# Optimization experiments

Measured on AMD Instinct MI355X. Metric: run time of the kernel, lower is better.

The kernel has to match this reference:

```python
import jax, jax.numpy as jnp
import numpy as np

N = 100000
E = 600000
D_IN, D_HID, D_OUT = 128, 128, 64


def setup_inputs() -> dict:
    key = jax.random.key(0)
    k1, k2, k3, k4 = jax.random.split(key, 4)
    x = jax.random.normal(k1, (N, D_IN), dtype=jnp.float32)
    edge_index = jax.random.randint(k2, (2, E), 0, N, dtype=jnp.int64)
    edge_weight = jnp.ones((E,), dtype=jnp.float32)
    W1 = jax.random.normal(k3, (D_IN, D_HID), dtype=jnp.float32) / np.sqrt(D_IN)
    b1 = jnp.zeros((D_HID,), dtype=jnp.float32)
    W2 = jax.random.normal(k4, (D_HID, D_OUT), dtype=jnp.float32) / np.sqrt(D_HID)
    b2 = jnp.zeros((D_OUT,), dtype=jnp.float32)
    return {"x": x, "edge_index": edge_index, "edge_weight": edge_weight,
            "W1": W1, "b1": b1, "W2": W2, "b2": b2}


def _gcn_conv(x, row, col, ew, W, b, n_nodes):
    # x: [N, d_in]; row/col/ew include self loops. PyG gcn_norm:
    # deg[i] = sum of ew over edges with target i; norm = d^-1/2[row]*ew*d^-1/2[col]
    deg = jax.ops.segment_sum(ew, col, num_segments=n_nodes)
    dinv = jnp.where(deg > 0, jax.lax.rsqrt(deg), 0.0)
    norm = dinv[row] * ew * dinv[col]  # [E+N]
    xw = x @ W  # dense transform first (d_out <= d_in path)
    msg = xw[row] * norm[:, None]  # gather + scale  [E+N, d_out]
    out = jax.ops.segment_sum(msg, col, num_segments=n_nodes)  # scatter-add
    return out + b


def reference(x, edge_index, edge_weight, W1, b1, W2, b2):
    n = x.shape[0]
    loops = jnp.arange(n, dtype=edge_index.dtype)
    row = jnp.concatenate([edge_index[0], loops])
    col = jnp.concatenate([edge_index[1], loops])
    ew = jnp.concatenate([edge_weight, jnp.ones((n,), dtype=edge_weight.dtype)])
    # dropout is identity in eval mode
    h = jax.nn.relu(_gcn_conv(x, row, col, ew, W1, b1, n))
    out = _gcn_conv(h, row, col, ew, W2, b2, n)
    return out
```

## Files before the change

kernel.cpp:

```cpp
#include <hip/hip_runtime.h>


constexpr int SCAN_BLOCKS = 256;

typedef __attribute__((ext_vector_type(8))) short short8;
typedef __attribute__((ext_vector_type(4))) float f32x4;

__device__ __forceinline__ ushort f2bf(float f) {
    unsigned u = __float_as_uint(f);
    return (ushort)((u + 0x7fffu + ((u >> 16) & 1u)) >> 16);
}
__device__ __forceinline__ float bf2f(ushort h) {
    return __uint_as_float((unsigned)h << 16);
}

__global__ __launch_bounds__(256, 2) void gemm1_kernel(
        const float* __restrict__ X, const float* __restrict__ W1,
        ushort* __restrict__ Ab, int N, int G,
        int* __restrict__ cnt, const float* __restrict__ W2,
        ushort* __restrict__ W2t) {
    __shared__ __align__(16) ushort sX[128 * 128];
    __shared__ __align__(16) ushort sW[128 * 128];
    const int tid = threadIdx.x;

    if (blockIdx.x >= G) {
        const int b = blockIdx.x - G;
        const int n4 = (N + 3) >> 2;
        const int nbz = (n4 + 255) / 256;
        if (b < nbz) {
            const int i = b * 256 + tid;
            if (i < n4) reinterpret_cast<int4*>(cnt)[i] = make_int4(0, 0, 0, 0);
        } else {
            const int o = (b - nbz) * 256 + tid;
            if (o < 64 * 128)
                W2t[o] = f2bf(W2[(size_t)(o & 127) * 64 + (o >> 7)]);
        }
        return;
    }

    const int base = blockIdx.x * 128;
    #pragma unroll
    for (int p = 0; p < 8; p++) {
        const int ch = p * 256 + tid;
        const int r = ch >> 4, cpos = ch & 15;
        const int grow = base + r;
        uint4 u = make_uint4(0, 0, 0, 0);
        if (grow < N) {
            const float* xp = X + (size_t)grow * 128 + cpos * 8;
            const float4 a = *reinterpret_cast<const float4*>(xp);
            const float4 c = *reinterpret_cast<const float4*>(xp + 4);
            u.x = (uint)f2bf(a.x) | ((uint)f2bf(a.y) << 16);
            u.y = (uint)f2bf(a.z) | ((uint)f2bf(a.w) << 16);
            u.z = (uint)f2bf(c.x) | ((uint)f2bf(c.y) << 16);
            u.w = (uint)f2bf(c.z) | ((uint)f2bf(c.w) << 16);
        }
        const int b = (cpos * 16) ^ ((r & 7) << 4);
        *reinterpret_cast<uint4*>(reinterpret_cast<char*>(sX) + r * 256 + b) = u;
    }
    #pragma unroll
    for (int p = 0; p < 8; p++) {
        const int ch = p * 256 + tid;
        const int c = ch & 127, kc = ch >> 7;
        const int k0 = kc * 8;
        float f[8];
        #pragma unroll
        for (int j = 0; j < 8; j++) f[j] = W1[(size_t)(k0 + j) * 128 + c];
        uint4 u;
        u.x = (uint)f2bf(f[0]) | ((uint)f2bf(f[1]) << 16);
        u.y = (uint)f2bf(f[2]) | ((uint)f2bf(f[3]) << 16);
        u.z = (uint)f2bf(f[4]) | ((uint)f2bf(f[5]) << 16);
        u.w = (uint)f2bf(f[6]) | ((uint)f2bf(f[7]) << 16);
        const int b = (k0 * 2) ^ ((c & 7) << 4);
        *reinterpret_cast<uint4*>(reinterpret_cast<char*>(sW) + c * 256 + b) = u;
    }
    __syncthreads();

    const int lane = tid & 63;
    const int wid = tid >> 6;
    const int wr = wid >> 1;
    const int wc = wid & 1;
    const int lr = lane & 15;
    const int g  = lane >> 4;

    f32x4 acc[4][4];
    #pragma unroll
    for (int i = 0; i < 4; i++)
        #pragma unroll
        for (int f = 0; f < 4; f++) acc[i][f] = (f32x4){0.f, 0.f, 0.f, 0.f};

    #pragma unroll
    for (int ks = 0; ks < 4; ks++) {
        const int koff = ks * 64 + g * 16;
        short8 a[4], b[4];
        #pragma unroll
        for (int i = 0; i < 4; i++) {
            const int r = wr * 64 + i * 16 + lr;
            a[i] = *reinterpret_cast<const short8*>(
                reinterpret_cast<const char*>(sX) + r * 256 + (koff ^ ((r & 7) << 4)));
        }
        #pragma unroll
        for (int f = 0; f < 4; f++) {
            const int c = wc * 64 + f * 16 + lr;
            b[f] = *reinterpret_cast<const short8*>(
                reinterpret_cast<const char*>(sW) + c * 256 + (koff ^ ((c & 7) << 4)));
        }
        #pragma unroll
        for (int i = 0; i < 4; i++)
            #pragma unroll
            for (int f = 0; f < 4; f++)
                acc[i][f] = __builtin_amdgcn_mfma_f32_16x16x32_bf16(a[i], b[f], acc[i][f], 0, 0, 0);
    }

    #pragma unroll
    for (int i = 0; i < 4; i++)
        #pragma unroll
        for (int reg = 0; reg < 4; reg++) {
            const int grow = base + wr * 64 + i * 16 + g * 4 + reg;
            if (grow < N)
                #pragma unroll
                for (int f = 0; f < 4; f++)
                    Ab[(size_t)grow * 128 + wc * 64 + f * 16 + lr] = f2bf(acc[i][f][reg]);
        }
}

__global__ void cnt_kernel(const int* __restrict__ col, int* __restrict__ cnt,
                           int* __restrict__ rank, int E) {
    const int T = gridDim.x * blockDim.x;
    for (int e = blockIdx.x * blockDim.x + threadIdx.x; e < E; e += T)
        rank[e] = atomicAdd(&cnt[col[e]], 1);
}

__global__ __launch_bounds__(256) void scan_part_kernel(
        const int* __restrict__ cnt, int* __restrict__ partial, int N) {
    const int T = SCAN_BLOCKS * 256;
    const int chunk = (N + T - 1) / T;
    const int j = blockIdx.x * 256 + threadIdx.x;
    const int s = j * chunk, e = min(s + chunk, N);
    int acc = 0;
    for (int i = s; i < e; i++) acc += cnt[i];
    __shared__ int red[256];
    red[threadIdx.x] = acc;
    __syncthreads();
    for (int off = 128; off > 0; off >>= 1) {
        if (threadIdx.x < off) red[threadIdx.x] += red[threadIdx.x + off];
        __syncthreads();
    }
    if (threadIdx.x == 0) partial[blockIdx.x] = red[0];
}

__global__ __launch_bounds__(256) void scan_write_kernel(
        const int* __restrict__ cnt, const int* __restrict__ partial,
        int* __restrict__ rowptr, int N, int E) {
    __shared__ int tp[256];
    __shared__ int sh[256];
    const int t = threadIdx.x;
    tp[t] = partial[t];
    __syncthreads();
    for (int off = 1; off < 256; off <<= 1) {
        int x = tp[t];
        int a = (t >= off) ? tp[t - off] : 0;
        __syncthreads();
        tp[t] = x + a;
        __syncthreads();
    }
    const int blockOff = (blockIdx.x == 0) ? 0 : tp[blockIdx.x - 1];
    const int T = SCAN_BLOCKS * 256;
    const int chunk = (N + T - 1) / T;
    const int j = blockIdx.x * 256 + t;
    const int s = j * chunk, e = min(s + chunk, N);
    int acc = 0;
    for (int i = s; i < e; i++) acc += cnt[i];
    sh[t] = acc;
    __syncthreads();
    for (int off = 1; off < 256; off <<= 1) {
        int x = sh[t];
        int a = (t >= off) ? sh[t - off] : 0;
        __syncthreads();
        sh[t] = x + a;
        __syncthreads();
    }
    int excl = blockOff + ((t == 0) ? 0 : sh[t - 1]);
    for (int i = s; i < e; i++) { rowptr[i] = excl; excl += cnt[i]; }
    if (j == 0) rowptr[N] = E;
}

__global__ void fill_kernel(const int* __restrict__ row, const int* __restrict__ col,
        const float* __restrict__ ew, const int* __restrict__ rowptr,
        const int* __restrict__ rank, int2* __restrict__ csr, int E) {
    int e = blockIdx.x * blockDim.x + threadIdx.x;
    if (e < E) {
        const int p = rowptr[col[e]] + rank[e];
        csr[p] = make_int2(row[e], __float_as_int(ew[e]));
    }
}

__global__ __launch_bounds__(256) void degsum_kernel(
        const int* __restrict__ rowptr, const int2* __restrict__ csr,
        float* __restrict__ dinv, int N) {
    const int n = blockIdx.x * blockDim.x + threadIdx.x;
    if (n >= N) return;
    const int e0 = rowptr[n], e1 = rowptr[n + 1];
    float d = 1.0f;
    for (int e = e0; e < e1; e++) d += __int_as_float(csr[e].y);
    dinv[n] = (d > 0.0f) ? rsqrtf(d) : 0.0f;
}

__global__ __launch_bounds__(256) void agg1_kernel(
        const int* __restrict__ rowptr, const int2* __restrict__ csr,
        const float* __restrict__ dinv,
        const ushort* __restrict__ src, const float* __restrict__ bias,
        ushort* __restrict__ dst, int N) {
    const int gid = blockIdx.x * 256 + threadIdx.x;
    const int c = gid >> 4;
    if (c >= N) return;
    const int lane = gid & 15;
    const float di = dinv[c];
    const float sl = di * di;
    float acc[8];
    {
        const short8 s8 = *reinterpret_cast<const short8*>(src + (size_t)c * 128 + lane * 8);
        #pragma unroll
        for (int j = 0; j < 8; j++) acc[j] = bf2f((ushort)s8[j]) * sl;
    }
    const int e0 = rowptr[c], e1 = rowptr[c + 1];
    int e = e0;
    for (; e + 4 <= e1; e += 4) {
        const int2 c0 = csr[e], c1 = csr[e + 1], c2 = csr[e + 2], c3 = csr[e + 3];
        const float w0 = __int_as_float(c0.y) * dinv[c0.x] * di;
        const float w1 = __int_as_float(c1.y) * dinv[c1.x] * di;
        const float w2 = __int_as_float(c2.y) * dinv[c2.x] * di;
        const float w3 = __int_as_float(c3.y) * dinv[c3.x] * di;
        const short8 v0 = *reinterpret_cast<const short8*>(src + (size_t)c0.x * 128 + lane * 8);
        const short8 v1 = *reinterpret_cast<const short8*>(src + (size_t)c1.x * 128 + lane * 8);
        const short8 v2 = *reinterpret_cast<const short8*>(src + (size_t)c2.x * 128 + lane * 8);
        const short8 v3 = *reinterpret_cast<const short8*>(src + (size_t)c3.x * 128 + lane * 8);
        #pragma unroll
        for (int j = 0; j < 8; j++)
            acc[j] += bf2f((ushort)v0[j]) * w0 + bf2f((ushort)v1[j]) * w1 +
                      bf2f((ushort)v2[j]) * w2 + bf2f((ushort)v3[j]) * w3;
    }
    for (; e < e1; e++) {
        const int2 ce = csr[e];
        const float w = __int_as_float(ce.y) * dinv[ce.x] * di;
        const short8 v = *reinterpret_cast<const short8*>(src + (size_t)ce.x * 128 + lane * 8);
        #pragma unroll
        for (int j = 0; j < 8; j++) acc[j] += bf2f((ushort)v[j]) * w;
    }
    const float4 b0 = reinterpret_cast<const float4*>(bias)[lane * 2];
    const float4 b1 = reinterpret_cast<const float4*>(bias)[lane * 2 + 1];
    acc[0] = fmaxf(acc[0] + b0.x, 0.f); acc[1] = fmaxf(acc[1] + b0.y, 0.f);
    acc[2] = fmaxf(acc[2] + b0.z, 0.f); acc[3] = fmaxf(acc[3] + b0.w, 0.f);
    acc[4] = fmaxf(acc[4] + b1.x, 0.f); acc[5] = fmaxf(acc[5] + b1.y, 0.f);
    acc[6] = fmaxf(acc[6] + b1.z, 0.f); acc[7] = fmaxf(acc[7] + b1.w, 0.f);
    uint4 o;
    o.x = (uint)f2bf(acc[0]) | ((uint)f2bf(acc[1]) << 16);
    o.y = (uint)f2bf(acc[2]) | ((uint)f2bf(acc[3]) << 16);
    o.z = (uint)f2bf(acc[4]) | ((uint)f2bf(acc[5]) << 16);
    o.w = (uint)f2bf(acc[6]) | ((uint)f2bf(acc[7]) << 16);
    *reinterpret_cast<uint4*>(dst + (size_t)c * 128 + lane * 8) = o;
}

__global__ __launch_bounds__(256, 2) void gemm2_kernel(
        const ushort* __restrict__ Xb, const ushort* __restrict__ Wt,
        ushort* __restrict__ Y, int N) {
    __shared__ __align__(16) ushort sX[128 * 128];
    __shared__ __align__(16) ushort sW[64 * 128];
    const int tid = threadIdx.x;
    const int base = blockIdx.x * 128;

    #pragma unroll
    for (int p = 0; p < 8; p++) {
        const int ch = p * 256 + tid;
        const int r = ch >> 4, cpos = ch & 15;
        const int grow = base + r;
        uint4 v = make_uint4(0, 0, 0, 0);
        if (grow < N)
            v = *reinterpret_cast<const uint4*>(Xb + (size_t)grow * 128 + cpos * 8);
        const int b = (cpos * 16) ^ ((r & 7) << 4);
        *reinterpret_cast<uint4*>(reinterpret_cast<char*>(sX) + r * 256 + b) = v;
    }
    #pragma unroll
    for (int p = 0; p < 4; p++) {
        const int ch = p * 256 + tid;
        const int r = ch >> 4, cpos = ch & 15;
        uint4 v = *reinterpret_cast<const uint4*>(Wt + (size_t)r * 128 + cpos * 8);
        const int b = (cpos * 16) ^ ((r & 7) << 4);
        *reinterpret_cast<uint4*>(reinterpret_cast<char*>(sW) + r * 256 + b) = v;
    }
    __syncthreads();

    const int lane = tid & 63;
    const int wid = tid >> 6;
    const int lr = lane & 15;
    const int g  = lane >> 4;

    f32x4 acc[2][4];
    #pragma unroll
    for (int i = 0; i < 2; i++)
        #pragma unroll
        for (int f = 0; f < 4; f++) acc[i][f] = (f32x4){0.f, 0.f, 0.f, 0.f};

    #pragma unroll
    for (int ks = 0; ks < 4; ks++) {
        const int koff = ks * 64 + g * 16;
        short8 a[2], b[4];
        #pragma unroll
        for (int i = 0; i < 2; i++) {
            const int r = wid * 32 + i * 16 + lr;
            a[i] = *reinterpret_cast<const short8*>(
                reinterpret_cast<const char*>(sX) + r * 256 + (koff ^ ((r & 7) << 4)));
        }
        #pragma unroll
        for (int f = 0; f < 4; f++) {
            const int c = f * 16 + lr;
            b[f] = *reinterpret_cast<const short8*>(
                reinterpret_cast<const char*>(sW) + c * 256 + (koff ^ ((c & 7) << 4)));
        }
        #pragma unroll
        for (int i = 0; i < 2; i++)
            #pragma unroll
            for (int f = 0; f < 4; f++)
                acc[i][f] = __builtin_amdgcn_mfma_f32_16x16x32_bf16(a[i], b[f], acc[i][f], 0, 0, 0);
    }

    #pragma unroll
    for (int i = 0; i < 2; i++)
        #pragma unroll
        for (int reg = 0; reg < 4; reg++) {
            const int grow = base + wid * 32 + i * 16 + g * 4 + reg;
            if (grow < N)
                #pragma unroll
                for (int f = 0; f < 4; f++)
                    Y[(size_t)grow * 64 + f * 16 + lr] = f2bf(acc[i][f][reg]);
        }
}

__global__ __launch_bounds__(256) void agg2_kernel(
        const int* __restrict__ rowptr, const int2* __restrict__ csr,
        const float* __restrict__ dinv,
        const ushort* __restrict__ src, const float* __restrict__ bias,
        float* __restrict__ dst, int N) {
    const int gid = blockIdx.x * 256 + threadIdx.x;
    const int c = gid >> 3;
    if (c >= N) return;
    const int lane = gid & 7;
    const float di = dinv[c];
    const float sl = di * di;
    float acc[8];
    {
        const short8 s8 = *reinterpret_cast<const short8*>(src + (size_t)c * 64 + lane * 8);
        #pragma unroll
        for (int j = 0; j < 8; j++) acc[j] = bf2f((ushort)s8[j]) * sl;
    }
    const int e0 = rowptr[c], e1 = rowptr[c + 1];
    int e = e0;
    for (; e + 4 <= e1; e += 4) {
        const int2 c0 = csr[e], c1 = csr[e + 1], c2 = csr[e + 2], c3 = csr[e + 3];
        const float w0 = __int_as_float(c0.y) * dinv[c0.x] * di;
        const float w1 = __int_as_float(c1.y) * dinv[c1.x] * di;
        const float w2 = __int_as_float(c2.y) * dinv[c2.x] * di;
        const float w3 = __int_as_float(c3.y) * dinv[c3.x] * di;
        const short8 v0 = *reinterpret_cast<const short8*>(src + (size_t)c0.x * 64 + lane * 8);
        const short8 v1 = *reinterpret_cast<const short8*>(src + (size_t)c1.x * 64 + lane * 8);
        const short8 v2 = *reinterpret_cast<const short8*>(src + (size_t)c2.x * 64 + lane * 8);
        const short8 v3 = *reinterpret_cast<const short8*>(src + (size_t)c3.x * 64 + lane * 8);
        #pragma unroll
        for (int j = 0; j < 8; j++)
            acc[j] += bf2f((ushort)v0[j]) * w0 + bf2f((ushort)v1[j]) * w1 +
                      bf2f((ushort)v2[j]) * w2 + bf2f((ushort)v3[j]) * w3;
    }
    for (; e < e1; e++) {
        const int2 ce = csr[e];
        const float w = __int_as_float(ce.y) * dinv[ce.x] * di;
        const short8 v = *reinterpret_cast<const short8*>(src + (size_t)ce.x * 64 + lane * 8);
        #pragma unroll
        for (int j = 0; j < 8; j++) acc[j] += bf2f((ushort)v[j]) * w;
    }
    const float4 b0 = reinterpret_cast<const float4*>(bias)[lane * 2];
    const float4 b1 = reinterpret_cast<const float4*>(bias)[lane * 2 + 1];
    float* dp = dst + (size_t)c * 64 + lane * 8;
    *reinterpret_cast<float4*>(dp) =
        make_float4(acc[0] + b0.x, acc[1] + b0.y, acc[2] + b0.z, acc[3] + b0.w);
    *reinterpret_cast<float4*>(dp + 4) =
        make_float4(acc[4] + b1.x, acc[5] + b1.y, acc[6] + b1.z, acc[7] + b1.w);
}

extern "C" void kernel_launch(void* const* d_in, const int* in_sizes, int n_in,
                              void* d_out, int out_size, void* d_ws, size_t ws_size,
                              hipStream_t stream) {
    const float* x  = (const float*)d_in[0];
    const int*   ei = (const int*)d_in[1];
    const float* ew = (const float*)d_in[2];
    const float* W1 = (const float*)d_in[3];
    const float* b1 = (const float*)d_in[4];
    const float* W2 = (const float*)d_in[5];
    const float* b2 = (const float*)d_in[6];
    const int N = in_sizes[0] / 128;
    const int E = in_sizes[1] / 2;
    const int* row = ei;
    const int* col = ei + E;

    char* w = (char*)d_ws;
    float* dinv = (float*)w;                 w += (size_t)N * 4;
    ushort* Ab  = (ushort*)w;                w += (size_t)N * 256;
    ushort* Hb  = (ushort*)w;                w += (size_t)N * 256;
    ushort* Gb  = (ushort*)w;                w += (size_t)N * 128;
    ushort* W2t = (ushort*)w;                w += 64 * 128 * 2;
    int* cnt    = (int*)w;                   w += (size_t)N * 4 + 16;
    int* rowptr = (int*)w;                   w += (size_t)(N + 8) * 4;
    int* partial= (int*)w;                   w += 2048 * 4;
    int* rank   = (int*)w;                   w += (size_t)E * 4;
    int2* csr   = (int2*)w;
    float* out  = (float*)d_out;

    const int ntiles = (N + 127) / 128;
    const int nbz = (((N + 3) >> 2) + 255) / 256;

    gemm1_kernel<<<ntiles + nbz + 32, 256, 0, stream>>>(x, W1, Ab, N, ntiles,
                                                        cnt, W2, W2t);
    cnt_kernel<<<(E / 8 + 255) / 256, 256, 0, stream>>>(col, cnt, rank, E);
    scan_part_kernel<<<SCAN_BLOCKS, 256, 0, stream>>>(cnt, partial, N);
    scan_write_kernel<<<SCAN_BLOCKS, 256, 0, stream>>>(cnt, partial, rowptr, N, E);
    fill_kernel<<<(E + 255) / 256, 256, 0, stream>>>(row, col, ew, rowptr, rank, csr, E);
    degsum_kernel<<<(N + 255) / 256, 256, 0, stream>>>(rowptr, csr, dinv, N);
    agg1_kernel<<<(N * 16 + 255) / 256, 256, 0, stream>>>(rowptr, csr, dinv, Ab, b1, Hb, N);
    gemm2_kernel<<<ntiles, 256, 0, stream>>>(Hb, W2t, Gb, N);
    agg2_kernel<<<(N * 8 + 255) / 256, 256, 0, stream>>>(rowptr, csr, dinv, Gb, b2, out, N);
}
```

Measured before the change: 135.6 us.

## Fuse edge counting into GEMM1 launch and merge scan passes with grid barrier

Moves cnt zeroing and W2 conversion into a small prep kernel so the atomic edge counting can run inside the GEMM1 launch as extra blocks, overlapping it with the dense transform. Merges the two scan kernels into one that uses a global atomic flag as a grid-wide barrier, which removes a launch and the repeated cnt reads. Vectorises the fill and count kernels to process four edges per thread. The spin barrier depends on all 256 scan blocks being resident at once, and the flag is reset by the zeroing pass (cnt+N).

```diff
diff --git a/kernel.cpp b/kernel.cpp
--- a/kernel.cpp
+++ b/kernel.cpp
@@ -14,26 +14,44 @@
     return __uint_as_float((unsigned)h << 16);
 }
 
-__global__ __launch_bounds__(256, 2) void gemm1_kernel(
+__global__ __launch_bounds__(256) void prep_kernel(
+        int* __restrict__ cnt, int N,
+        const float* __restrict__ W2, ushort* __restrict__ W2t) {
+    const int n4 = (N >> 2) + 1;
+    const int nbz = (n4 + 255) / 256;
+    int b = blockIdx.x;
+    if (b < nbz) {
+        const int i = b * 256 + threadIdx.x;
+        if (i < n4) reinterpret_cast<int4*>(cnt)[i] = make_int4(0, 0, 0, 0);
+        return;
+    }
+    b -= nbz;
+    const int o = b * 256 + threadIdx.x;
+    if (o < 64 * 128)
+        W2t[o] = f2bf(W2[(size_t)(o & 127) * 64 + (o >> 7)]);
+}
+
+__global__ __launch_bounds__(256, 2) void combo_kernel(
         const float* __restrict__ X, const float* __restrict__ W1,
         ushort* __restrict__ Ab, int N, int G,
-        int* __restrict__ cnt, const float* __restrict__ W2,
-        ushort* __restrict__ W2t) {
+        const int* __restrict__ col, int* __restrict__ cnt,
+        int* __restrict__ rank, int E) {
     __shared__ __align__(16) ushort sX[128 * 128];
     __shared__ __align__(16) ushort sW[128 * 128];
     const int tid = threadIdx.x;
 
     if (blockIdx.x >= G) {
-        const int b = blockIdx.x - G;
-        const int n4 = (N + 3) >> 2;
-        const int nbz = (n4 + 255) / 256;
-        if (b < nbz) {
-            const int i = b * 256 + tid;
-            if (i < n4) reinterpret_cast<int4*>(cnt)[i] = make_int4(0, 0, 0, 0);
+        const int e4 = ((blockIdx.x - G) * 256 + tid) * 4;
+        if (e4 + 3 < E) {
+            const int4 c4 = *reinterpret_cast<const int4*>(col + e4);
+            int4 r4;
+            r4.x = atomicAdd(&cnt[c4.x], 1);
+            r4.y = atomicAdd(&cnt[c4.y], 1);
+            r4.z = atomicAdd(&cnt[c4.z], 1);
+            r4.w = atomicAdd(&cnt[c4.w], 1);
+            *reinterpret_cast<int4*>(rank + e4) = r4;
         } else {
-            const int o = (b - nbz) * 256 + tid;
-            if (o < 64 * 128)
-                W2t[o] = f2bf(W2[(size_t)(o & 127) * 64 + (o >> 7)]);
+            for (int e = e4; e < E; e++) rank[e] = atomicAdd(&cnt[col[e]], 1);
         }
         return;
     }
@@ -123,38 +141,41 @@
         }
 }
 
-__global__ void cnt_kernel(const int* __restrict__ col, int* __restrict__ cnt,
-                           int* __restrict__ rank, int E) {
-    const int T = gridDim.x * blockDim.x;
-    for (int e = blockIdx.x * blockDim.x + threadIdx.x; e < E; e += T)
-        rank[e] = atomicAdd(&cnt[col[e]], 1);
-}
-
-__global__ __launch_bounds__(256) void scan_part_kernel(
-        const int* __restrict__ cnt, int* __restrict__ partial, int N) {
+__global__ __launch_bounds__(256) void scan_kernel(
+        const int* __restrict__ cnt, int* __restrict__ rowptr,
+        int* __restrict__ partial, int* __restrict__ flag, int N, int E) {
+    const int t = threadIdx.x, b = blockIdx.x;
     const int T = SCAN_BLOCKS * 256;
     const int chunk = (N + T - 1) / T;
-    const int j = blockIdx.x * 256 + threadIdx.x;
-    const int s = j * chunk, e = min(s + chunk, N);
+    const int j = b * 256 + t;
+    const int s = min(j * chunk, N), e = min(s + chunk, N);
     int acc = 0;
     for (int i = s; i < e; i++) acc += cnt[i];
-    __shared__ int red[256];
-    red[threadIdx.x] = acc;
-    __syncthreads();
-    for (int off = 128; off > 0; off >>= 1) {
-        if (threadIdx.x < off) red[threadIdx.x] += red[threadIdx.x + off];
+
+    __shared__ int sh[256];
+    sh[t] = acc;
+    __syncthreads();
+    for (int off = 1; off < 256; off <<= 1) {
+        int x = sh[t];
+        int a = (t >= off) ? sh[t - off] : 0;
         __syncthreads();
-    }
-    if (threadIdx.x == 0) partial[blockIdx.x] = red[0];
-}
-
-__global__ __launch_bounds__(256) void scan_write_kernel(
-        const int* __restrict__ cnt, const int* __restrict__ partial,
-        int* __restrict__ rowptr, int N, int E) {
+        sh[t] = x + a;
+        __syncthreads();
+    }
+    const int thr_excl = sh[t] - acc;
+    if (t == 255) partial[b] = sh[255];
+    __syncthreads();
+    if (t == 0) {
+        __threadfence();
+        atomicAdd(flag, 1);
+        while (__hip_atomic_load(flag, __ATOMIC_RELAXED,
+                                 __HIP_MEMORY_SCOPE_AGENT) < SCAN_BLOCKS) {}
+    }
+    __syncthreads();
+
     __shared__ int tp[256];
-    __shared__ int sh[256];
-    const int t = threadIdx.x;
-    tp[t] = partial[t];
+    tp[t] = __hip_atomic_load(&partial[t], __ATOMIC_RELAXED,
+                              __HIP_MEMORY_SCOPE_AGENT);
     __syncthreads();
     for (int off = 1; off < 256; off <<= 1) {
         int x = tp[t];
@@ -163,34 +184,31 @@
         tp[t] = x + a;
         __syncthreads();
     }
-    const int blockOff = (blockIdx.x == 0) ? 0 : tp[blockIdx.x - 1];
-    const int T = SCAN_BLOCKS * 256;
-    const int chunk = (N + T - 1) / T;
-    const int j = blockIdx.x * 256 + t;
-    const int s = j * chunk, e = min(s + chunk, N);
-    int acc = 0;
-    for (int i = s; i < e; i++) acc += cnt[i];
-    sh[t] = acc;
-    __syncthreads();
-    for (int off = 1; off < 256; off <<= 1) {
-        int x = sh[t];
-        int a = (t >= off) ? sh[t - off] : 0;
-        __syncthreads();
-        sh[t] = x + a;
-        __syncthreads();
-    }
-    int excl = blockOff + ((t == 0) ? 0 : sh[t - 1]);
-    for (int i = s; i < e; i++) { rowptr[i] = excl; excl += cnt[i]; }
+    int run = ((b == 0) ? 0 : tp[b - 1]) + thr_excl;
+    for (int i = s; i < e; i++) { rowptr[i] = run; run += cnt[i]; }
     if (j == 0) rowptr[N] = E;
 }
 
 __global__ void fill_kernel(const int* __restrict__ row, const int* __restrict__ col,
         const float* __restrict__ ew, const int* __restrict__ rowptr,
         const int* __restrict__ rank, int2* __restrict__ csr, int E) {
-    int e = blockIdx.x * blockDim.x + threadIdx.x;
-    if (e < E) {
-        const int p = rowptr[col[e]] + rank[e];
-        csr[p] = make_int2(row[e], __float_as_int(ew[e]));
+    const int e4 = (blockIdx.x * blockDim.x + threadIdx.x) * 4;
+    if (e4 + 3 < E) {
+        const int4 c4 = *reinterpret_cast<const int4*>(col + e4);
+        const int4 r4 = *reinterpret_cast<const int4*>(row + e4);
+        const int4 w4 = *reinterpret_cast<const int4*>((const int*)ew + e4);
+        const int4 k4 = *reinterpret_cast<const int4*>(rank + e4);
+        const int p0 = rowptr[c4.x] + k4.x;
+        const int p1 = rowptr[c4.y] + k4.y;
+        const int p2 = rowptr[c4.z] + k4.z;
+        const int p3 = rowptr[c4.w] + k4.w;
+        csr[p0] = make_int2(r4.x, w4.x);
+        csr[p1] = make_int2(r4.y, w4.y);
+        csr[p2] = make_int2(r4.z, w4.z);
+        csr[p3] = make_int2(r4.w, w4.w);
+    } else {
+        for (int e = e4; e < E; e++)
+            csr[rowptr[col[e]] + rank[e]] = make_int2(row[e], __float_as_int(ew[e]));
     }
 }
 
@@ -412,16 +430,17 @@
     int* rank   = (int*)w;                   w += (size_t)E * 4;
     int2* csr   = (int2*)w;
     float* out  = (float*)d_out;
+    int* flag   = cnt + N;
 
     const int ntiles = (N + 127) / 128;
-    const int nbz = (((N + 3) >> 2) + 255) / 256;
-
-    gemm1_kernel<<<ntiles + nbz + 32, 256, 0, stream>>>(x, W1, Ab, N, ntiles,
-                                                        cnt, W2, W2t);
-    cnt_kernel<<<(E / 8 + 255) / 256, 256, 0, stream>>>(col, cnt, rank, E);
-    scan_part_kernel<<<SCAN_BLOCKS, 256, 0, stream>>>(cnt, partial, N);
-    scan_write_kernel<<<SCAN_BLOCKS, 256, 0, stream>>>(cnt, partial, rowptr, N, E);
-    fill_kernel<<<(E + 255) / 256, 256, 0, stream>>>(row, col, ew, rowptr, rank, csr, E);
+    const int nbz = ((N >> 2) + 1 + 255) / 256;
+    const int eb4 = (E / 4 + 255) / 256;
+
+    prep_kernel<<<nbz + 32, 256, 0, stream>>>(cnt, N, W2, W2t);
+    combo_kernel<<<ntiles + eb4, 256, 0, stream>>>(x, W1, Ab, N, ntiles,
+                                                   col, cnt, rank, E);
+    scan_kernel<<<SCAN_BLOCKS, 256, 0, stream>>>(cnt, rowptr, partial, flag, N, E);
+    fill_kernel<<<eb4, 256, 0, stream>>>(row, col, ew, rowptr, rank, csr, E);
     degsum_kernel<<<(N + 255) / 256, 256, 0, stream>>>(rowptr, csr, dinv, N);
     agg1_kernel<<<(N * 16 + 255) / 256, 256, 0, stream>>>(rowptr, csr, dinv, Ab, b1, Hb, N);
     gemm2_kernel<<<ntiles, 256, 0, stream>>>(Hb, W2t, Gb, N);
```

Measured after the change: 142.7 us. 5.2% more time.
